# Kernel optimization log

Hardware: AMD Instinct MI355X
Metric: run time of the kernel (lower is better)

Reference implementation:

```python
import jax, jax.numpy as jnp
import numpy as np

BLOCK_LEN = 64

def setup_inputs() -> dict:
    key = jax.random.key(0)
    k1, k2, k3 = jax.random.split(key, 3)
    b, T, h, p, n = 2, 8192, 16, 64, 64
    X = jax.random.normal(k1, (b, T, h), dtype=jnp.float32)  # placeholder reuse avoided below
    X = jax.random.normal(k1, (b, T, h, p), dtype=jnp.float32)
    # A kept negative (as in Mamba/SSD) so exp(decay) stays bounded and the
    # inter-chunk product of exp(A_last) does not overflow.
    A = -jnp.abs(jax.random.normal(k2, (b, T, h), dtype=jnp.float32)) * 0.1
    B = jax.random.normal(k3, (b, T, h, n), dtype=jnp.float32)
    return {"X": X, "A": A, "B": B}


def reference(X, A, B):
    b, T, h, p = X.shape
    n = B.shape[-1]
    l = BLOCK_LEN
    c = T // l

    # [b, h, c, l] chunked A
    A_blocks = A.reshape(b, c, l, h).transpose(0, 3, 1, 2)
    A_cumsum = jnp.cumsum(A_blocks, axis=-1)          # s[i] = sum_{t<=i} a[t]
    A_last = A_cumsum[..., -1]                        # [b, h, c] total per chunk
    decay = jnp.exp(A_last[..., None] - A_cumsum)     # exp(S_total - s[i]) [b,h,c,l]

    X_blocks = X.reshape(b, c, l, h, p)
    B_blocks = B.reshape(b, c, l, h, n)

    # intra-chunk states: sum_l decay * outer(X, B) -> [b, c, h, p, n]
    states = jnp.einsum('bclhn,bhcl,bclhp->bchpn', B_blocks, decay, X_blocks)

    # inter-chunk recurrence: s_{k+1} = exp(A_last[...,k]) * s_k + states[:,k]
    init = jnp.zeros((b, h, p, n), dtype=jnp.float32)
    states_c = jnp.moveaxis(states, 1, 0)             # [c, b, h, p, n]
    A_last_c = jnp.moveaxis(A_last, 2, 0)             # [c, b, h]

    def step(s, inp):
        st, al = inp
        return jnp.exp(al)[..., None, None] * s + st, None

    final_states, _ = jax.lax.scan(step, init, (states_c, A_last_c))
    return final_states  # [b, h, p, n]
```

## Files before the change

kernel.cpp:

```cpp
#include <hip/hip_runtime.h>

#define B_SZ 2
#define T_SZ 8192
#define H_SZ 16
#define P_SZ 64
#define N_SZ 64
#define L_SZ 64
#define C_SZ (T_SZ / L_SZ)
#define SKIP_THRESH (-30.0f)

__global__ void __launch_bounds__(256) k_chunk_sums(const float* __restrict__ A,
                                                    float* __restrict__ cs) {
    int blk = blockIdx.x;
    int b = blk / C_SZ;
    int c = blk % C_SZ;
    __shared__ float a_sh[L_SZ * H_SZ];
    const float4* src =
        (const float4*)(A + ((size_t)b * T_SZ + (size_t)c * L_SZ) * H_SZ);
    int tid = threadIdx.x;
    ((float4*)a_sh)[tid] = src[tid];
    __syncthreads();
    if (tid < H_SZ) {
        float s = 0.f;
        #pragma unroll 8
        for (int i = 0; i < L_SZ; ++i) s += a_sh[i * H_SZ + tid];
        cs[((size_t)b * H_SZ + tid) * C_SZ + c] = s;
    }
}

__global__ void k_suffix(const float* __restrict__ cs, float* __restrict__ saf) {
    int bh = blockIdx.x;
    if (threadIdx.x == 0) {
        float acc = 0.f;
        for (int k = C_SZ - 1; k >= 0; --k) {
            saf[(size_t)bh * C_SZ + k] = acc;
            acc += cs[(size_t)bh * C_SZ + k];
        }
    }
}

__global__ void __launch_bounds__(256) k_states(const float* __restrict__ X,
                                                const float* __restrict__ A,
                                                const float* __restrict__ Bm,
                                                const float* __restrict__ saf,
                                                float* __restrict__ out) {
    const int c = blockIdx.x;
    const int h = blockIdx.y;
    const int b = blockIdx.z;

    const float safter = saf[((size_t)b * H_SZ + h) * C_SZ + c];
    if (safter < SKIP_THRESH) return;

    __shared__ float a_sh[L_SZ];
    __shared__ float w_sh[L_SZ];
    __shared__ float xw_sh[L_SZ * P_SZ];
    __shared__ float b_sh[L_SZ * N_SZ];

    const int tid = threadIdx.x;
    const size_t base_t = (size_t)b * T_SZ + (size_t)c * L_SZ;

    const float* Xp = X + (base_t * H_SZ + h) * (size_t)P_SZ;
    const float* Bp = Bm + (base_t * H_SZ + h) * (size_t)N_SZ;
    float4 xr[4], br[4];
    #pragma unroll
    for (int k = 0; k < 4; ++k) {
        int idx = tid + k * 256;
        int row = idx >> 4;
        int col = idx & 15;
        xr[k] = *(const float4*)(Xp + (size_t)row * (H_SZ * P_SZ) + col * 4);
        br[k] = *(const float4*)(Bp + (size_t)row * (H_SZ * N_SZ) + col * 4);
    }

    if (tid < L_SZ) a_sh[tid] = A[(base_t + tid) * H_SZ + h];
    __syncthreads();
    if (tid == 0) {
        float acc = 0.f;
        for (int i = L_SZ - 1; i >= 0; --i) {
            w_sh[i] = acc;
            acc += a_sh[i];
        }
    }
    __syncthreads();
    if (tid < L_SZ) w_sh[tid] = expf(w_sh[tid] + safter);
    __syncthreads();

    #pragma unroll
    for (int k = 0; k < 4; ++k) {
        int idx = tid + k * 256;
        int row = idx >> 4;
        float wv = w_sh[row];
        float4 xv = xr[k];
        xv.x *= wv; xv.y *= wv; xv.z *= wv; xv.w *= wv;
        ((float4*)xw_sh)[idx] = xv;
        ((float4*)b_sh)[idx] = br[k];
    }
    __syncthreads();

    const int pi = (tid >> 4) << 2;
    const int ni = (tid & 15) << 2;
    float acc00 = 0.f, acc01 = 0.f, acc02 = 0.f, acc03 = 0.f;
    float acc10 = 0.f, acc11 = 0.f, acc12 = 0.f, acc13 = 0.f;
    float acc20 = 0.f, acc21 = 0.f, acc22 = 0.f, acc23 = 0.f;
    float acc30 = 0.f, acc31 = 0.f, acc32 = 0.f, acc33 = 0.f;
    #pragma unroll 4
    for (int t = 0; t < L_SZ; ++t) {
        float4 xv = *(const float4*)(xw_sh + t * P_SZ + pi);
        float4 bv = *(const float4*)(b_sh + t * N_SZ + ni);
        acc00 += xv.x * bv.x; acc01 += xv.x * bv.y; acc02 += xv.x * bv.z; acc03 += xv.x * bv.w;
        acc10 += xv.y * bv.x; acc11 += xv.y * bv.y; acc12 += xv.y * bv.z; acc13 += xv.y * bv.w;
        acc20 += xv.z * bv.x; acc21 += xv.z * bv.y; acc22 += xv.z * bv.z; acc23 += xv.z * bv.w;
        acc30 += xv.w * bv.x; acc31 += xv.w * bv.y; acc32 += xv.w * bv.z; acc33 += xv.w * bv.w;
    }

    float* op = out + (((size_t)b * H_SZ + h) * P_SZ) * N_SZ;
    atomicAdd(op + (pi + 0) * N_SZ + ni + 0, acc00);
    atomicAdd(op + (pi + 0) * N_SZ + ni + 1, acc01);
    atomicAdd(op + (pi + 0) * N_SZ + ni + 2, acc02);
    atomicAdd(op + (pi + 0) * N_SZ + ni + 3, acc03);
    atomicAdd(op + (pi + 1) * N_SZ + ni + 0, acc10);
    atomicAdd(op + (pi + 1) * N_SZ + ni + 1, acc11);
    atomicAdd(op + (pi + 1) * N_SZ + ni + 2, acc12);
    atomicAdd(op + (pi + 1) * N_SZ + ni + 3, acc13);
    atomicAdd(op + (pi + 2) * N_SZ + ni + 0, acc20);
    atomicAdd(op + (pi + 2) * N_SZ + ni + 1, acc21);
    atomicAdd(op + (pi + 2) * N_SZ + ni + 2, acc22);
    atomicAdd(op + (pi + 2) * N_SZ + ni + 3, acc23);
    atomicAdd(op + (pi + 3) * N_SZ + ni + 0, acc30);
    atomicAdd(op + (pi + 3) * N_SZ + ni + 1, acc31);
    atomicAdd(op + (pi + 3) * N_SZ + ni + 2, acc32);
    atomicAdd(op + (pi + 3) * N_SZ + ni + 3, acc33);
}

extern "C" void kernel_launch(void* const* d_in, const int* in_sizes, int n_in,
                              void* d_out, int out_size, void* d_ws, size_t ws_size,
                              hipStream_t stream) {
    const float* X  = (const float*)d_in[0];
    const float* A  = (const float*)d_in[1];
    const float* Bm = (const float*)d_in[2];
    float* out = (float*)d_out;

    float* cs  = (float*)d_ws;
    float* saf = cs + (size_t)B_SZ * H_SZ * C_SZ;

    hipMemsetAsync(d_out, 0, (size_t)out_size * sizeof(float), stream);

    k_chunk_sums<<<B_SZ * C_SZ, 256, 0, stream>>>(A, cs);
    k_suffix<<<B_SZ * H_SZ, 64, 0, stream>>>(cs, saf);

    dim3 grid(C_SZ, H_SZ, B_SZ);
    k_states<<<grid, 256, 0, stream>>>(X, A, Bm, saf, out);
}
```

Before: 146.2 us.

## Fuse output zeroing and suffix scan into prep and main kernels

Drops the separate memset and the single-threaded suffix-sum kernel. The prep kernel now also zeroes the output, and each main block rebuilds its own suffix sum with a shared-memory plus wavefront-shuffle reduction over the chunk totals. The serial intra-chunk cumulative sum becomes a 64-lane shuffle scan using fast __expf. This cuts two launches and a serial dependency chain, at the cost of redundant reduction work in every block.

```diff
diff --git a/kernel.cpp b/kernel.cpp
--- a/kernel.cpp
+++ b/kernel.cpp
@@ -9,54 +9,65 @@
 #define C_SZ (T_SZ / L_SZ)
 #define SKIP_THRESH (-30.0f)
 
-__global__ void __launch_bounds__(256) k_chunk_sums(const float* __restrict__ A,
-                                                    float* __restrict__ cs) {
-    int blk = blockIdx.x;
-    int b = blk / C_SZ;
-    int c = blk % C_SZ;
+__global__ void __launch_bounds__(256) k_prep(const float* __restrict__ A,
+                                              float* __restrict__ cs,
+                                              float* __restrict__ out) {
+    const int blk = blockIdx.x;
+    const int b = blk / C_SZ;
+    const int c = blk % C_SZ;
+    const int tid = threadIdx.x;
     __shared__ float a_sh[L_SZ * H_SZ];
     const float4* src =
         (const float4*)(A + ((size_t)b * T_SZ + (size_t)c * L_SZ) * H_SZ);
-    int tid = threadIdx.x;
     ((float4*)a_sh)[tid] = src[tid];
+
+    if (tid < 128) {
+        float4 z; z.x = z.y = z.z = z.w = 0.f;
+        ((float4*)out)[(size_t)blk * 128 + tid] = z;
+    }
     __syncthreads();
     if (tid < H_SZ) {
         float s = 0.f;
-        #pragma unroll 8
+        #pragma unroll
         for (int i = 0; i < L_SZ; ++i) s += a_sh[i * H_SZ + tid];
         cs[((size_t)b * H_SZ + tid) * C_SZ + c] = s;
     }
 }
 
-__global__ void k_suffix(const float* __restrict__ cs, float* __restrict__ saf) {
-    int bh = blockIdx.x;
-    if (threadIdx.x == 0) {
-        float acc = 0.f;
-        for (int k = C_SZ - 1; k >= 0; --k) {
-            saf[(size_t)bh * C_SZ + k] = acc;
-            acc += cs[(size_t)bh * C_SZ + k];
-        }
-    }
-}
-
-__global__ void __launch_bounds__(256) k_states(const float* __restrict__ X,
-                                                const float* __restrict__ A,
-                                                const float* __restrict__ Bm,
-                                                const float* __restrict__ saf,
-                                                float* __restrict__ out) {
+__global__ void __launch_bounds__(256) k_main(const float* __restrict__ X,
+                                              const float* __restrict__ A,
+                                              const float* __restrict__ Bm,
+                                              const float* __restrict__ cs,
+                                              float* __restrict__ out) {
     const int c = blockIdx.x;
     const int h = blockIdx.y;
     const int b = blockIdx.z;
+    const int bh = b * H_SZ + h;
+    const int tid = threadIdx.x;
 
-    const float safter = saf[((size_t)b * H_SZ + h) * C_SZ + c];
-    if (safter < SKIP_THRESH) return;
-
-    __shared__ float a_sh[L_SZ];
+    __shared__ float red[128];
+    __shared__ float s_saf;
     __shared__ float w_sh[L_SZ];
     __shared__ float xw_sh[L_SZ * P_SZ];
     __shared__ float b_sh[L_SZ * N_SZ];
 
-    const int tid = threadIdx.x;
+    if (tid < 128)
+        red[tid] = (tid > c) ? cs[(size_t)bh * C_SZ + tid] : 0.f;
+    __syncthreads();
+    if (tid < 64) {
+        float x = red[tid] + red[tid + 64];
+        x += __shfl_down(x, 32);
+        x += __shfl_down(x, 16);
+        x += __shfl_down(x, 8);
+        x += __shfl_down(x, 4);
+        x += __shfl_down(x, 2);
+        x += __shfl_down(x, 1);
+        if (tid == 0) s_saf = x;
+    }
+    __syncthreads();
+    const float safter = s_saf;
+    if (safter < SKIP_THRESH) return;
+
     const size_t base_t = (size_t)b * T_SZ + (size_t)c * L_SZ;
 
     const float* Xp = X + (base_t * H_SZ + h) * (size_t)P_SZ;
@@ -71,17 +82,16 @@
         br[k] = *(const float4*)(Bp + (size_t)row * (H_SZ * N_SZ) + col * 4);
     }
 
-    if (tid < L_SZ) a_sh[tid] = A[(base_t + tid) * H_SZ + h];
-    __syncthreads();
-    if (tid == 0) {
-        float acc = 0.f;
-        for (int i = L_SZ - 1; i >= 0; --i) {
-            w_sh[i] = acc;
-            acc += a_sh[i];
+    if (tid < 64) {
+        float incl = A[(base_t + tid) * H_SZ + h];
+        #pragma unroll
+        for (int off = 1; off < 64; off <<= 1) {
+            float y = __shfl_up(incl, off);
+            if (tid >= off) incl += y;
         }
+        float total = __shfl(incl, 63);
+        w_sh[tid] = __expf(total - incl + safter);
     }
-    __syncthreads();
-    if (tid < L_SZ) w_sh[tid] = expf(w_sh[tid] + safter);
     __syncthreads();
 
     #pragma unroll
@@ -139,14 +149,10 @@
     const float* Bm = (const float*)d_in[2];
     float* out = (float*)d_out;
 
-    float* cs  = (float*)d_ws;
-    float* saf = cs + (size_t)B_SZ * H_SZ * C_SZ;
+    float* cs = (float*)d_ws;
 
-    hipMemsetAsync(d_out, 0, (size_t)out_size * sizeof(float), stream);
-
-    k_chunk_sums<<<B_SZ * C_SZ, 256, 0, stream>>>(A, cs);
-    k_suffix<<<B_SZ * H_SZ, 64, 0, stream>>>(cs, saf);
+    k_prep<<<B_SZ * C_SZ, 256, 0, stream>>>(A, cs, out);
 
     dim3 grid(C_SZ, H_SZ, B_SZ);
-    k_states<<<grid, 256, 0, stream>>>(X, A, Bm, saf, out);
+    k_main<<<grid, 256, 0, stream>>>(X, A, Bm, cs, out);
 }
```

New measurement: 143.5 us. No clear change (-1.9%).
